# Performance work log

Hardware: AMD Instinct MI355X
Metric: run time of the kernel (lower is better)

Reference implementation:

```python
import jax, jax.numpy as jnp
import numpy as np

B, T, V, E, H, U = 32, 64, 32000, 300, 512, 512


def setup_inputs() -> dict:
    key = jax.random.key(0)
    ks = jax.random.split(key, 14)
    s = 0.05  # weight scale to keep gates in a sane range
    return {
        "trg_seq": jax.random.randint(ks[0], (B, T), 0, V, dtype=jnp.int32),
        "init_h": jax.random.normal(ks[1], (1, B, U), jnp.float32),
        "init_c": jax.random.normal(ks[2], (1, B, U), jnp.float32),
        "embedding": jax.random.normal(ks[3], (V, E), jnp.float32) * s,
        "Wh": jax.random.normal(ks[4], (H, U), jnp.float32) * s,
        "bh": jax.random.normal(ks[5], (H,), jnp.float32) * s,
        "Wc": jax.random.normal(ks[6], (H, U), jnp.float32) * s,
        "bc": jax.random.normal(ks[7], (H,), jnp.float32) * s,
        "W_ih": jax.random.normal(ks[8], (4 * H, E), jnp.float32) * s,
        "W_hh": jax.random.normal(ks[9], (4 * H, H), jnp.float32) * s,
        "b_ih": jax.random.normal(ks[10], (4 * H,), jnp.float32) * s,
        "b_hh": jax.random.normal(ks[11], (4 * H,), jnp.float32) * s,
        "W_logit": jax.random.normal(ks[12], (V, H), jnp.float32) * s,
        "b_logit": jax.random.normal(ks[13], (V,), jnp.float32) * s,
    }


def reference(trg_seq, init_h, init_c, embedding, Wh, bh, Wc, bc,
              W_ih, W_hh, b_ih, b_hh, W_logit, b_logit):
    # form_init: linear transform of encoder states -> LSTM initial h/c
    h0 = init_h[0] @ Wh.T + bh  # [B, H]
    c0 = init_c[0] @ Wc.T + bc  # [B, H]

    emb = embedding[trg_seq]                       # [B, T, E]
    x_gates = jnp.einsum('bte,ge->btg', emb, W_ih) + b_ih + b_hh  # [B, T, 4H]

    def step(carry, xg_t):
        h, c = carry
        gates = xg_t + h @ W_hh.T                  # [B, 4H]
        i, f, g, o = jnp.split(gates, 4, axis=-1)  # torch gate order i,f,g,o
        i, f, o = jax.nn.sigmoid(i), jax.nn.sigmoid(f), jax.nn.sigmoid(o)
        g = jnp.tanh(g)
        c = f * c + i * g
        h = o * jnp.tanh(c)
        return (h, c), h

    _, hs = jax.lax.scan(step, (h0, c0), x_gates.transpose(1, 0, 2))  # hs: [T, B, H]
    logits = jnp.tanh(hs) @ W_logit.T + b_logit    # [T, B, V]
    return logits.transpose(1, 0, 2)               # [B, T, V]
```

## Files before the change

kernel.cpp:

```cpp
#include <hip/hip_runtime.h>
#include <hip/hip_cooperative_groups.h>

typedef unsigned short u16;
typedef __attribute__((ext_vector_type(8))) unsigned short us8;
typedef __attribute__((ext_vector_type(8))) __bf16 bf16x8;
typedef __attribute__((ext_vector_type(4))) float f32x4;

#define B_ 32
#define T_ 64
#define V_ 32000
#define E_ 300
#define H_ 512
#define G4_ 2048
#define NBLK_ 32
#define NG_   224
#define NT_TILES 250
#define NM_TILES 16

__device__ __forceinline__ u16 f2b(float f){
  unsigned int x = __builtin_bit_cast(unsigned int, f);
  unsigned int r = (x + 0x7FFFu + ((x >> 16) & 1u)) >> 16;
  return (u16)r;
}
__device__ __forceinline__ float sigm(float x){ return 1.0f/(1.0f+expf(-x)); }

__device__ __forceinline__ void gload16(const u16* g, u16* l){
  __builtin_amdgcn_global_load_lds(
      (const __attribute__((address_space(1))) void*)g,
      (__attribute__((address_space(3))) void*)l, 16, 0, 0);
}

__global__ __launch_bounds__(256) void k_init(
    const float* __restrict__ init_h, const float* __restrict__ init_c,
    const float* __restrict__ Wh, const float* __restrict__ bh,
    const float* __restrict__ Wc, const float* __restrict__ bc,
    float* __restrict__ h0out, float* __restrict__ c0out,
    unsigned int* __restrict__ flag)
{
  if (blockIdx.x == 0){ flag[threadIdx.x] = 0u; flag[threadIdx.x + 256] = 0u; }
  int idx = blockIdx.x*blockDim.x + threadIdx.x;
  int sel = idx >> 14;
  int r = idx & 16383;
  int b = r >> 9, j = r & 511;
  const float* x = (sel ? init_c : init_h) + b*H_;
  const float* w = (sel ? Wc : Wh) + (size_t)j*H_;
  const float* bias = sel ? bc : bh;
  float acc = 0.f;
  for (int k = 0; k < H_; k += 8){
    f32x4 x0 = *(const f32x4*)(x + k), x1 = *(const f32x4*)(x + k + 4);
    f32x4 w0 = *(const f32x4*)(w + k), w1 = *(const f32x4*)(w + k + 4);
    acc += x0[0]*w0[0] + x0[1]*w0[1] + x0[2]*w0[2] + x0[3]*w0[3];
    acc += x1[0]*w1[0] + x1[1]*w1[1] + x1[2]*w1[2] + x1[3]*w1[3];
  }
  acc += bias[j];
  (sel ? c0out : h0out)[b*H_ + j] = acc;
}

__global__ __launch_bounds__(256) void k_cvt(
    const float* __restrict__ W, u16* __restrict__ W16)
{
  size_t i = ((size_t)blockIdx.x*256 + threadIdx.x)*8;
  f32x4 a = *(const f32x4*)(W + i);
  f32x4 b = *(const f32x4*)(W + i + 4);
  us8 u;
  u[0]=f2b(a[0]); u[1]=f2b(a[1]); u[2]=f2b(a[2]); u[3]=f2b(a[3]);
  u[4]=f2b(b[0]); u[5]=f2b(b[1]); u[6]=f2b(b[2]); u[7]=f2b(b[3]);
  *(us8*)(W16 + i) = u;
}

__global__ __launch_bounds__(256) void k_xgates(
    const float* __restrict__ emb, const float* __restrict__ Wih,
    const int* __restrict__ trg, const float* __restrict__ bih,
    const float* __restrict__ bhh, float* __restrict__ xg)
{
  __shared__ u16 As[128][40];
  __shared__ u16 Bs[128][40];
  const int bn0 = blockIdx.x*128, bm0 = blockIdx.y*128;
  const int tid = threadIdx.x;
  const int w = tid>>6, lane = tid&63;
  const int wr = w>>1, wc = w&1, lr = lane&15, lk = lane>>4;
  const int srow = tid>>1, half = tid&1;
  const int R = bm0 + srow;
  const int tt = R>>5, bb = R&31;
  const int token = trg[bb*T_ + tt];
  const float* arow = emb + (size_t)token*E_;
  const float* brow = Wih + (size_t)(bn0+srow)*E_;
  f32x4 acc[4][4] = {};
  for (int k0 = 0; k0 < E_; k0 += 32){
    int cbase = k0 + half*16;
    if (k0 + 32 <= E_){
      f32x4 a0=*(const f32x4*)(arow+cbase),    a1=*(const f32x4*)(arow+cbase+4);
      f32x4 a2=*(const f32x4*)(arow+cbase+8),  a3=*(const f32x4*)(arow+cbase+12);
      f32x4 b0=*(const f32x4*)(brow+cbase),    b1=*(const f32x4*)(brow+cbase+4);
      f32x4 b2=*(const f32x4*)(brow+cbase+8),  b3=*(const f32x4*)(brow+cbase+12);
      us8 ua, ub;
      ua[0]=f2b(a0[0]); ua[1]=f2b(a0[1]); ua[2]=f2b(a0[2]); ua[3]=f2b(a0[3]);
      ua[4]=f2b(a1[0]); ua[5]=f2b(a1[1]); ua[6]=f2b(a1[2]); ua[7]=f2b(a1[3]);
      ub[0]=f2b(a2[0]); ub[1]=f2b(a2[1]); ub[2]=f2b(a2[2]); ub[3]=f2b(a2[3]);
      ub[4]=f2b(a3[0]); ub[5]=f2b(a3[1]); ub[6]=f2b(a3[2]); ub[7]=f2b(a3[3]);
      *(us8*)&As[srow][half*16]   = ua;
      *(us8*)&As[srow][half*16+8] = ub;
      us8 va, vb;
      va[0]=f2b(b0[0]); va[1]=f2b(b0[1]); va[2]=f2b(b0[2]); va[3]=f2b(b0[3]);
      va[4]=f2b(b1[0]); va[5]=f2b(b1[1]); va[6]=f2b(b1[2]); va[7]=f2b(b1[3]);
      vb[0]=f2b(b2[0]); vb[1]=f2b(b2[1]); vb[2]=f2b(b2[2]); vb[3]=f2b(b2[3]);
      vb[4]=f2b(b3[0]); vb[5]=f2b(b3[1]); vb[6]=f2b(b3[2]); vb[7]=f2b(b3[3]);
      *(us8*)&Bs[srow][half*16]   = va;
      *(us8*)&Bs[srow][half*16+8] = vb;
    } else {
      for (int i = 0; i < 16; i++){
        int c = cbase + i;
        As[srow][half*16+i] = (c < E_) ? f2b(arow[c]) : (u16)0;
        Bs[srow][half*16+i] = (c < E_) ? f2b(brow[c]) : (u16)0;
      }
    }
    __syncthreads();
    bf16x8 af[4], bfr[4];
    #pragma unroll
    for (int m = 0; m < 4; m++) af[m] = *(const bf16x8*)&As[wr*64 + m*16 + lr][lk*8];
    #pragma unroll
    for (int n = 0; n < 4; n++) bfr[n] = *(const bf16x8*)&Bs[wc*64 + n*16 + lr][lk*8];
    #pragma unroll
    for (int m = 0; m < 4; m++)
      #pragma unroll
      for (int n = 0; n < 4; n++)
        acc[m][n] = __builtin_amdgcn_mfma_f32_16x16x32_bf16(af[m], bfr[n], acc[m][n], 0, 0, 0);
    __syncthreads();
  }
  #pragma unroll
  for (int n = 0; n < 4; n++){
    int col = bn0 + wc*64 + n*16 + lr;
    float bv = bih[col] + bhh[col];
    #pragma unroll
    for (int m = 0; m < 4; m++){
      #pragma unroll
      for (int i = 0; i < 4; i++){
        int row = bm0 + wr*64 + m*16 + lk*4 + i;
        xg[(size_t)row*G4_ + col] = acc[m][n][i] + bv;
      }
    }
  }
}

__global__ __launch_bounds__(512) void k_mega(
    const float* __restrict__ Whh, const float* __restrict__ xg,
    const float* __restrict__ h0, const float* __restrict__ c0,
    u16* __restrict__ h_g, u16* __restrict__ A_buf,
    unsigned int* __restrict__ flag,
    const u16* __restrict__ W16, const float* __restrict__ bias,
    float* __restrict__ out)
{
  __shared__ __align__(16) char smem[41472];
  const int tid = threadIdx.x;

  if (blockIdx.x < NBLK_){
    u16 (*hl)[520] = (u16(*)[520])smem;
    float (*gb)[32][16] = (float(*)[32][16])(smem + 33280);
    const int bj = blockIdx.x;
    const int wv = tid >> 6, lane = tid & 63;
    const int g = wv >> 1, m = wv & 1;
    const int lr = lane & 15, lk = lane >> 4;

    bf16x8 bw[16];
    {
      const float* wsrc = Whh + (size_t)(g*H_ + bj*16 + lr)*H_;
      #pragma unroll
      for (int ks = 0; ks < 16; ks++){
        f32x4 w0 = *(const f32x4*)(wsrc + ks*32 + lk*8);
        f32x4 w1 = *(const f32x4*)(wsrc + ks*32 + lk*8 + 4);
        us8 u;
        u[0]=f2b(w0[0]); u[1]=f2b(w0[1]); u[2]=f2b(w0[2]); u[3]=f2b(w0[3]);
        u[4]=f2b(w1[0]); u[5]=f2b(w1[1]); u[6]=f2b(w1[2]); u[7]=f2b(w1[3]);
        bw[ks] = __builtin_bit_cast(bf16x8, u);
      }
    }
    const int ub = tid >> 4, uj = tid & 15;
    float c_reg = c0[ub*H_ + bj*16 + uj];

    {
      int r = tid >> 4, seg = tid & 15;
      const float* src = h0 + r*H_ + seg*32;
      #pragma unroll
      for (int q = 0; q < 4; q++){
        f32x4 v0 = *(const f32x4*)(src + q*8);
        f32x4 v1 = *(const f32x4*)(src + q*8 + 4);
        us8 u;
        u[0]=f2b(v0[0]); u[1]=f2b(v0[1]); u[2]=f2b(v0[2]); u[3]=f2b(v0[3]);
        u[4]=f2b(v1[0]); u[5]=f2b(v1[1]); u[6]=f2b(v1[2]); u[7]=f2b(v1[3]);
        *(us8*)&hl[r][seg*32 + q*8] = u;
      }
    }
    __syncthreads();

    for (int t = 0; t < T_; t++){
      const float* xr = xg + (size_t)t*(B_*G4_) + ub*G4_ + bj*16 + uj;
      float x0 = xr[0*H_], x1 = xr[1*H_], x2 = xr[2*H_], x3 = xr[3*H_];

      f32x4 acc = {0.f, 0.f, 0.f, 0.f};
      #pragma unroll
      for (int ks = 0; ks < 16; ks++){
        bf16x8 a = *(const bf16x8*)&hl[m*16 + lr][ks*32 + lk*8];
        acc = __builtin_amdgcn_mfma_f32_16x16x32_bf16(a, bw[ks], acc, 0, 0, 0);
      }
      #pragma unroll
      for (int i = 0; i < 4; i++)
        gb[g][m*16 + lk*4 + i][lr] = acc[i];
      __syncthreads();

      float gi = sigm(gb[0][ub][uj] + x0);
      float gf = sigm(gb[1][ub][uj] + x1);
      float gg = tanhf(gb[2][ub][uj] + x2);
      float go = sigm(gb[3][ub][uj] + x3);
      c_reg = gf*c_reg + gi*gg;
      float h = go * tanhf(c_reg);
      int p = (t+1) & 1;
      h_g[p*(B_*H_) + bj*(B_*16) + tid] = f2b(h);

      __syncthreads();
      if (t < T_-1 && tid == 0)
        __hip_atomic_store(&flag[bj*16], (unsigned)(t+1),
                           __ATOMIC_RELEASE, __HIP_MEMORY_SCOPE_AGENT);

      A_buf[(size_t)t*(B_*H_) + ub*H_ + bj*16 + uj] = f2b(tanhf(h));
      if (t == T_-1) break;

      if (tid < 64){
        unsigned want = (unsigned)(t+1), guard = 0;
        while (__hip_atomic_load(&flag[(tid&31)*16], __ATOMIC_ACQUIRE,
                                 __HIP_MEMORY_SCOPE_AGENT) < want
               && guard < (1u<<18)) { __builtin_amdgcn_s_sleep(1); ++guard; }
      }
      __syncthreads();

      {
        int r = tid >> 4, seg = tid & 15;
        const u16* hb = h_g + p*(B_*H_);
        const u16* p0 = hb + (seg*2)  *(B_*16) + r*16;
        const u16* p1 = hb + (seg*2+1)*(B_*16) + r*16;
        us8 v0 = *(const us8*)(p0);
        us8 v1 = *(const us8*)(p0 + 8);
        us8 v2 = *(const us8*)(p1);
        us8 v3 = *(const us8*)(p1 + 8);
        *(us8*)&hl[r][seg*32]      = v0;
        *(us8*)&hl[r][seg*32 + 8]  = v1;
        *(us8*)&hl[r][seg*32 + 16] = v2;
        *(us8*)&hl[r][seg*32 + 24] = v3;
      }
      __syncthreads();
    }
    __syncthreads();
    if (tid == 0)
      __hip_atomic_store(&flag[bj*16], 65u,
                         __ATOMIC_RELEASE, __HIP_MEMORY_SCOPE_AGENT);
  } else {
    u16* As = (u16*)smem;
    u16* Bs = (u16*)(smem + 16384);
    const int w = tid>>6, lane = tid&63;
    const int wr = w & 1, wc = w >> 1;
    const int lr = lane&15, lk = lane>>4;
    const int r0 = w*8 + (lane>>3);
    const int r1 = 64 + r0;
    const int c0b = ((lane&7)*16) ^ ((r0&7)<<4);
    const int c1b = ((lane&7)*16) ^ ((r1&7)<<4);
    u16* adst0 = &As[(w*8)*64];
    u16* adst1 = &As[(64 + w*8)*64];
    u16* bdst0 = &Bs[(w*8)*64];
    u16* bdst1 = &Bs[(64 + w*8)*64];

    int prev_want = -1;
    for (int tile = (int)blockIdx.x - NBLK_; tile < NM_TILES*NT_TILES; tile += NG_){
      const int mt = tile / NT_TILES;
      const int nt = tile - mt*NT_TILES;
      const int bm0 = mt*128, bn0 = nt*128;
      const unsigned want = (mt < 15) ? (unsigned)(4*mt + 5) : 65u;
      if ((int)want != prev_want){
        if (tid < 64){
          unsigned guard = 0;
          for (;;){
            unsigned v = __hip_atomic_load(&flag[(tid&31)*16], __ATOMIC_RELAXED,
                                           __HIP_MEMORY_SCOPE_AGENT);
            if (__all(v >= want) || guard > (1u<<20)) break;
            __builtin_amdgcn_s_sleep(8); ++guard;
          }
          __builtin_amdgcn_fence(__ATOMIC_ACQUIRE, "agent");
        }
        prev_want = (int)want;
      }
      __syncthreads();

      const u16* a0p = A_buf + (size_t)(bm0+r0)*H_ + (c0b>>1);
      const u16* a1p = A_buf + (size_t)(bm0+r1)*H_ + (c1b>>1);
      const u16* b0p = W16   + (size_t)(bn0+r0)*H_ + (c0b>>1);
      const u16* b1p = W16   + (size_t)(bn0+r1)*H_ + (c1b>>1);
      f32x4 acc[4][2] = {};
      for (int k0 = 0; k0 < H_; k0 += 64){
        gload16(a0p + k0, adst0);
        gload16(a1p + k0, adst1);
        gload16(b0p + k0, bdst0);
        gload16(b1p + k0, bdst1);
        __syncthreads();
        #pragma unroll
        for (int s = 0; s < 2; s++){
          bf16x8 af[4], bfr[2];
          #pragma unroll
          for (int m = 0; m < 4; m++){
            int row = wr*64 + m*16 + lr;
            af[m] = *(const bf16x8*)((const char*)As + row*128
                       + ((s*64 + lk*16) ^ ((row&7)<<4)));
          }
          #pragma unroll
          for (int n = 0; n < 2; n++){
            int row = wc*32 + n*16 + lr;
            bfr[n] = *(const bf16x8*)((const char*)Bs + row*128
                       + ((s*64 + lk*16) ^ ((row&7)<<4)));
          }
          #pragma unroll
          for (int m = 0; m < 4; m++)
            #pragma unroll
            for (int n = 0; n < 2; n++)
              acc[m][n] = __builtin_amdgcn_mfma_f32_16x16x32_bf16(af[m], bfr[n], acc[m][n], 0, 0, 0);
        }
        __syncthreads();
      }
      #pragma unroll
      for (int n = 0; n < 2; n++){
        int col = bn0 + wc*32 + n*16 + lr;
        float bv = bias[col];
        #pragma unroll
        for (int m = 0; m < 4; m++){
          #pragma unroll
          for (int i = 0; i < 4; i++){
            int row = bm0 + wr*64 + m*16 + lk*4 + i;
            int t = row>>5, b = row&31;
            __builtin_nontemporal_store(acc[m][n][i] + bv,
                &out[(size_t)b*((size_t)T_*V_) + (size_t)t*V_ + col]);
          }
        }
      }
    }
  }
}

__global__ __launch_bounds__(512) void k_scan(
    const float* __restrict__ Whh, const float* __restrict__ xg,
    const float* __restrict__ h0, const float* __restrict__ c0,
    u16* __restrict__ h_g, u16* __restrict__ A_buf,
    unsigned int* __restrict__ flag)
{
  __shared__ u16 hl[32][520];
  __shared__ float gb[4][32][16];
  const int bj = blockIdx.x;
  const int tid = threadIdx.x;
  const int wv = tid >> 6, lane = tid & 63;
  const int g = wv >> 1, m = wv & 1;
  const int lr = lane & 15, lk = lane >> 4;
  bf16x8 bw[16];
  {
    const float* wsrc = Whh + (size_t)(g*H_ + bj*16 + lr)*H_;
    #pragma unroll
    for (int ks = 0; ks < 16; ks++){
      f32x4 w0 = *(const f32x4*)(wsrc + ks*32 + lk*8);
      f32x4 w1 = *(const f32x4*)(wsrc + ks*32 + lk*8 + 4);
      us8 u;
      u[0]=f2b(w0[0]); u[1]=f2b(w0[1]); u[2]=f2b(w0[2]); u[3]=f2b(w0[3]);
      u[4]=f2b(w1[0]); u[5]=f2b(w1[1]); u[6]=f2b(w1[2]); u[7]=f2b(w1[3]);
      bw[ks] = __builtin_bit_cast(bf16x8, u);
    }
  }
  const int ub = tid >> 4, uj = tid & 15;
  float c_reg = c0[ub*H_ + bj*16 + uj];
  {
    int r = tid >> 4, seg = tid & 15;
    const float* src = h0 + r*H_ + seg*32;
    #pragma unroll
    for (int q = 0; q < 4; q++){
      f32x4 v0 = *(const f32x4*)(src + q*8);
      f32x4 v1 = *(const f32x4*)(src + q*8 + 4);
      us8 u;
      u[0]=f2b(v0[0]); u[1]=f2b(v0[1]); u[2]=f2b(v0[2]); u[3]=f2b(v0[3]);
      u[4]=f2b(v1[0]); u[5]=f2b(v1[1]); u[6]=f2b(v1[2]); u[7]=f2b(v1[3]);
      *(us8*)&hl[r][seg*32 + q*8] = u;
    }
  }
  __syncthreads();
  for (int t = 0; t < T_; t++){
    const float* xr = xg + (size_t)t*(B_*G4_) + ub*G4_ + bj*16 + uj;
    float x0 = xr[0*H_], x1 = xr[1*H_], x2 = xr[2*H_], x3 = xr[3*H_];
    f32x4 acc = {0.f, 0.f, 0.f, 0.f};
    #pragma unroll
    for (int ks = 0; ks < 16; ks++){
      bf16x8 a = *(const bf16x8*)&hl[m*16 + lr][ks*32 + lk*8];
      acc = __builtin_amdgcn_mfma_f32_16x16x32_bf16(a, bw[ks], acc, 0, 0, 0);
    }
    #pragma unroll
    for (int i = 0; i < 4; i++)
      gb[g][m*16 + lk*4 + i][lr] = acc[i];
    __syncthreads();
    float gi = sigm(gb[0][ub][uj] + x0);
    float gf = sigm(gb[1][ub][uj] + x1);
    float gg = tanhf(gb[2][ub][uj] + x2);
    float go = sigm(gb[3][ub][uj] + x3);
    c_reg = gf*c_reg + gi*gg;
    float h = go * tanhf(c_reg);
    int p = (t+1) & 1;
    h_g[p*(B_*H_) + bj*(B_*16) + tid] = f2b(h);
    __syncthreads();
    if (t < T_-1 && tid == 0)
      __hip_atomic_store(&flag[bj*16], (unsigned)(t+1),
                         __ATOMIC_RELEASE, __HIP_MEMORY_SCOPE_AGENT);
    A_buf[(size_t)t*(B_*H_) + ub*H_ + bj*16 + uj] = f2b(tanhf(h));
    if (t == T_-1) break;
    if (tid < 64){
      unsigned want = (unsigned)(t+1), guard = 0;
      while (__hip_atomic_load(&flag[(tid&31)*16], __ATOMIC_ACQUIRE,
                               __HIP_MEMORY_SCOPE_AGENT) < want
             && guard < (1u<<18)) { __builtin_amdgcn_s_sleep(1); ++guard; }
    }
    __syncthreads();
    {
      int r = tid >> 4, seg = tid & 15;
      const u16* hb = h_g + p*(B_*H_);
      const u16* p0 = hb + (seg*2)  *(B_*16) + r*16;
      const u16* p1 = hb + (seg*2+1)*(B_*16) + r*16;
      us8 v0 = *(const us8*)(p0);
      us8 v1 = *(const us8*)(p0 + 8);
      us8 v2 = *(const us8*)(p1);
      us8 v3 = *(const us8*)(p1 + 8);
      *(us8*)&hl[r][seg*32]      = v0;
      *(us8*)&hl[r][seg*32 + 8]  = v1;
      *(us8*)&hl[r][seg*32 + 16] = v2;
      *(us8*)&hl[r][seg*32 + 24] = v3;
    }
    __syncthreads();
  }
}

__global__ __launch_bounds__(256) void k_logits16(
    const u16* __restrict__ A, const u16* __restrict__ W16,
    const float* __restrict__ bias, float* __restrict__ out)
{
  __shared__ u16 As[128*32];
  __shared__ u16 Bs[128*32];
  int bid = blockIdx.y*16 + blockIdx.x;
  int nbid = (bid & 7)*500 + (bid >> 3);
  const int bm0 = (nbid & 15)*128;
  const int bn0 = (nbid >> 4)*128;
  const int tid = threadIdx.x;
  const int w = tid>>6, lane = tid&63;
  const int wr = w>>1, wc = w&1, lr = lane&15, lk = lane>>4;
  const int srow = w*32 + (lane>>2);
  const int cb   = ((lane&3)*16) ^ (((srow>>1)&3)<<4);
  const u16* aptr = A   + (size_t)(bm0+srow)*H_ + (cb>>1);
  const u16* bptr = W16 + (size_t)(bn0+srow)*H_ + (cb>>1);
  u16* adst0 = &As[(w*32)*32];
  u16* adst1 = &As[(w*32+16)*32];
  u16* bdst0 = &Bs[(w*32)*32];
  u16* bdst1 = &Bs[(w*32+16)*32];
  f32x4 acc[4][4] = {};
  for (int k0 = 0; k0 < H_; k0 += 32){
    gload16(aptr + k0,          adst0);
    gload16(aptr + k0 + 16*H_,  adst1);
    gload16(bptr + k0,          bdst0);
    gload16(bptr + k0 + 16*H_,  bdst1);
    __syncthreads();
    bf16x8 af[4], bfr[4];
    #pragma unroll
    for (int m = 0; m < 4; m++){
      int row = wr*64 + m*16 + lr;
      af[m] = *(const bf16x8*)((const char*)As + row*64 + ((lk*16) ^ (((row>>1)&3)<<4)));
    }
    #pragma unroll
    for (int n = 0; n < 4; n++){
      int row = wc*64 + n*16 + lr;
      bfr[n] = *(const bf16x8*)((const char*)Bs + row*64 + ((lk*16) ^ (((row>>1)&3)<<4)));
    }
    #pragma unroll
    for (int m = 0; m < 4; m++)
      #pragma unroll
      for (int n = 0; n < 4; n++)
        acc[m][n] = __builtin_amdgcn_mfma_f32_16x16x32_bf16(af[m], bfr[n], acc[m][n], 0, 0, 0);
    __syncthreads();
  }
  #pragma unroll
  for (int n = 0; n < 4; n++){
    int col = bn0 + wc*64 + n*16 + lr;
    float bv = bias[col];
    #pragma unroll
    for (int m = 0; m < 4; m++){
      #pragma unroll
      for (int i = 0; i < 4; i++){
        int row = bm0 + wr*64 + m*16 + lk*4 + i;
        int t = row>>5, b = row&31;
        __builtin_nontemporal_store(acc[m][n][i] + bv,
            &out[(size_t)b*((size_t)T_*V_) + (size_t)t*V_ + col]);
      }
    }
  }
}

__global__ __launch_bounds__(256) void k_logits(
    const u16* __restrict__ A, const float* __restrict__ W,
    const float* __restrict__ bias, float* __restrict__ out)
{
  __shared__ u16 As[128][40];
  __shared__ u16 Bs[128][40];
  const int bm0 = blockIdx.x*128, bn0 = blockIdx.y*128;
  const int tid = threadIdx.x;
  const int w = tid>>6, lane = tid&63;
  const int wr = w>>1, wc = w&1, lr = lane&15, lk = lane>>4;
  const int srow = tid>>1, half = tid&1;
  const u16*   arow = A + (size_t)(bm0+srow)*H_;
  const float* brow = W + (size_t)(bn0+srow)*H_;
  f32x4 acc[4][4] = {};
  for (int k0 = 0; k0 < H_; k0 += 32){
    us8 a0 = *(const us8*)(arow + k0 + half*16);
    us8 a1 = *(const us8*)(arow + k0 + half*16 + 8);
    f32x4 b0 = *(const f32x4*)(brow + k0 + half*16);
    f32x4 b1 = *(const f32x4*)(brow + k0 + half*16 + 4);
    f32x4 b2 = *(const f32x4*)(brow + k0 + half*16 + 8);
    f32x4 b3 = *(const f32x4*)(brow + k0 + half*16 + 12);
    *(us8*)&As[srow][half*16]   = a0;
    *(us8*)&As[srow][half*16+8] = a1;
    us8 vb0, vb1;
    vb0[0]=f2b(b0[0]); vb0[1]=f2b(b0[1]); vb0[2]=f2b(b0[2]); vb0[3]=f2b(b0[3]);
    vb0[4]=f2b(b1[0]); vb0[5]=f2b(b1[1]); vb0[6]=f2b(b1[2]); vb0[7]=f2b(b1[3]);
    vb1[0]=f2b(b2[0]); vb1[1]=f2b(b2[1]); vb1[2]=f2b(b2[2]); vb1[3]=f2b(b2[3]);
    vb1[4]=f2b(b3[0]); vb1[5]=f2b(b3[1]); vb1[6]=f2b(b3[2]); vb1[7]=f2b(b3[3]);
    *(us8*)&Bs[srow][half*16]   = vb0;
    *(us8*)&Bs[srow][half*16+8] = vb1;
    __syncthreads();
    bf16x8 af[4], bfr[4];
    #pragma unroll
    for (int m = 0; m < 4; m++) af[m] = *(const bf16x8*)&As[wr*64 + m*16 + lr][lk*8];
    #pragma unroll
    for (int n = 0; n < 4; n++) bfr[n] = *(const bf16x8*)&Bs[wc*64 + n*16 + lr][lk*8];
    #pragma unroll
    for (int m = 0; m < 4; m++)
      #pragma unroll
      for (int n = 0; n < 4; n++)
        acc[m][n] = __builtin_amdgcn_mfma_f32_16x16x32_bf16(af[m], bfr[n], acc[m][n], 0, 0, 0);
    __syncthreads();
  }
  #pragma unroll
  for (int n = 0; n < 4; n++){
    int col = bn0 + wc*64 + n*16 + lr;
    float bv = bias[col];
    #pragma unroll
    for (int m = 0; m < 4; m++){
      #pragma unroll
      for (int i = 0; i < 4; i++){
        int row = bm0 + wr*64 + m*16 + lk*4 + i;
        int t = row>>5, b = row&31;
        out[(size_t)b*((size_t)T_*V_) + (size_t)t*V_ + col] = acc[m][n][i] + bv;
      }
    }
  }
}

extern "C" void kernel_launch(void* const* d_in, const int* in_sizes, int n_in,
                              void* d_out, int out_size, void* d_ws, size_t ws_size,
                              hipStream_t stream)
{
  const int*   trg    = (const int*)d_in[0];
  const float* init_h = (const float*)d_in[1];
  const float* init_c = (const float*)d_in[2];
  const float* emb    = (const float*)d_in[3];
  const float* Wh     = (const float*)d_in[4];
  const float* bh     = (const float*)d_in[5];
  const float* Wc     = (const float*)d_in[6];
  const float* bc     = (const float*)d_in[7];
  const float* Wih    = (const float*)d_in[8];
  const float* Whh    = (const float*)d_in[9];
  const float* bih    = (const float*)d_in[10];
  const float* bhh    = (const float*)d_in[11];
  const float* Wlogit = (const float*)d_in[12];
  const float* blogit = (const float*)d_in[13];
  float* out = (float*)d_out;

  char* ws = (char*)d_ws;
  float*        xg    = (float*)(ws);
  float*        h0    = (float*)(ws + 16777216);
  float*        c0    = (float*)(ws + 16842752);
  u16*          A_buf = (u16*)  (ws + 16908288);
  u16*          h_g   = (u16*)  (ws + 19005440);
  unsigned int* flag  = (unsigned int*)(ws + 19136512);
  u16*          W16   = (u16*)  (ws + 19138560);
  const size_t need_w16 = 19138560ull + 32768000ull;
  const bool use_w16 = (ws_size >= need_w16);

  hipLaunchKernelGGL(k_init, dim3(128), dim3(256), 0, stream,
                     init_h, init_c, Wh, bh, Wc, bc, h0, c0, flag);
  if (use_w16)
    hipLaunchKernelGGL(k_cvt, dim3((V_*H_)/(256*8)), dim3(256), 0, stream,
                       Wlogit, W16);
  hipLaunchKernelGGL(k_xgates, dim3(16, 16), dim3(256), 0, stream,
                     emb, Wih, trg, bih, bhh, xg);
  if (use_w16){
    void* args[] = { (void*)&Whh, (void*)&xg, (void*)&h0, (void*)&c0,
                     (void*)&h_g, (void*)&A_buf, (void*)&flag,
                     (void*)&W16, (void*)&blogit, (void*)&out };
    hipError_t merr = hipLaunchCooperativeKernel((void*)k_mega,
                          dim3(NBLK_ + NG_), dim3(512), args, 0, stream);
    if (merr != hipSuccess){
      void* sargs[] = { (void*)&Whh, (void*)&xg, (void*)&h0, (void*)&c0,
                        (void*)&h_g, (void*)&A_buf, (void*)&flag };
      hipLaunchCooperativeKernel((void*)k_scan, dim3(NBLK_), dim3(512),
                                 sargs, 0, stream);
      hipLaunchKernelGGL(k_logits16, dim3(16, 250), dim3(256), 0, stream,
                         A_buf, W16, blogit, out);
    }
  } else {
    void* args[] = { (void*)&Whh, (void*)&xg, (void*)&h0, (void*)&c0,
                     (void*)&h_g, (void*)&A_buf, (void*)&flag };
    hipLaunchCooperativeKernel((void*)k_scan, dim3(NBLK_), dim3(512), args, 0, stream);
    hipLaunchKernelGGL(k_logits, dim3(16, 250), dim3(256), 0, stream,
                       A_buf, Wlogit, blogit, out);
  }
}
```

Before: 439.5 us.

## Fuse weight conversion into xgates launch and pair M-tiles per logits tile

Folds the fp32-to-bf16 conversion of W_logit into the x-gates kernel as extra blocks, removing one kernel launch and letting the two independent jobs run concurrently. In the fused scan/logits megakernel, each consumer block now handles two consecutive M-tiles for the same N-tile. This keeps the W16 tile hot in cache and halves the tile-scheduling loop count. Pairing M-tiles can delay the start of the second tile's work until its scan flag is ready, which reduces how evenly work is spread across blocks.

```diff
diff --git a/kernel.cpp b/kernel.cpp
--- a/kernel.cpp
+++ b/kernel.cpp
@@ -56,27 +56,27 @@
   (sel ? c0out : h0out)[b*H_ + j] = acc;
 }
 
-__global__ __launch_bounds__(256) void k_cvt(
-    const float* __restrict__ W, u16* __restrict__ W16)
-{
-  size_t i = ((size_t)blockIdx.x*256 + threadIdx.x)*8;
-  f32x4 a = *(const f32x4*)(W + i);
-  f32x4 b = *(const f32x4*)(W + i + 4);
-  us8 u;
-  u[0]=f2b(a[0]); u[1]=f2b(a[1]); u[2]=f2b(a[2]); u[3]=f2b(a[3]);
-  u[4]=f2b(b[0]); u[5]=f2b(b[1]); u[6]=f2b(b[2]); u[7]=f2b(b[3]);
-  *(us8*)(W16 + i) = u;
-}
-
 __global__ __launch_bounds__(256) void k_xgates(
     const float* __restrict__ emb, const float* __restrict__ Wih,
     const int* __restrict__ trg, const float* __restrict__ bih,
-    const float* __restrict__ bhh, float* __restrict__ xg)
+    const float* __restrict__ bhh, float* __restrict__ xg,
+    const float* __restrict__ Wlogit, u16* __restrict__ W16)
 {
+  const int bid = blockIdx.x;
+  const int tid = threadIdx.x;
+  if (bid >= 256){
+    size_t i = ((size_t)(bid - 256)*256 + tid)*8;
+    f32x4 a = *(const f32x4*)(Wlogit + i);
+    f32x4 b = *(const f32x4*)(Wlogit + i + 4);
+    us8 u;
+    u[0]=f2b(a[0]); u[1]=f2b(a[1]); u[2]=f2b(a[2]); u[3]=f2b(a[3]);
+    u[4]=f2b(b[0]); u[5]=f2b(b[1]); u[6]=f2b(b[2]); u[7]=f2b(b[3]);
+    *(us8*)(W16 + i) = u;
+    return;
+  }
   __shared__ u16 As[128][40];
   __shared__ u16 Bs[128][40];
-  const int bn0 = blockIdx.x*128, bm0 = blockIdx.y*128;
-  const int tid = threadIdx.x;
+  const int bn0 = (bid & 15)*128, bm0 = (bid >> 4)*128;
   const int w = tid>>6, lane = tid&63;
   const int wr = w>>1, wc = w&1, lr = lane&15, lk = lane>>4;
   const int srow = tid>>1, half = tid&1;
@@ -268,72 +268,77 @@
     u16* bdst1 = &Bs[(64 + w*8)*64];
 
     int prev_want = -1;
-    for (int tile = (int)blockIdx.x - NBLK_; tile < NM_TILES*NT_TILES; tile += NG_){
-      const int mt = tile / NT_TILES;
-      const int nt = tile - mt*NT_TILES;
-      const int bm0 = mt*128, bn0 = nt*128;
-      const unsigned want = (mt < 15) ? (unsigned)(4*mt + 5) : 65u;
-      if ((int)want != prev_want){
-        if (tid < 64){
-          unsigned guard = 0;
-          for (;;){
-            unsigned v = __hip_atomic_load(&flag[(tid&31)*16], __ATOMIC_RELAXED,
-                                           __HIP_MEMORY_SCOPE_AGENT);
-            if (__all(v >= want) || guard > (1u<<20)) break;
-            __builtin_amdgcn_s_sleep(8); ++guard;
+    for (int pt = (int)blockIdx.x - NBLK_; pt < 8*NT_TILES; pt += NG_){
+      const int mt2 = pt / NT_TILES;
+      const int nt  = pt - mt2*NT_TILES;
+      const int bn0 = nt*128;
+      const u16* b0p = W16 + (size_t)(bn0+r0)*H_ + (c0b>>1);
+      const u16* b1p = W16 + (size_t)(bn0+r1)*H_ + (c1b>>1);
+      #pragma unroll
+      for (int hh = 0; hh < 2; hh++){
+        const int mt = 2*mt2 + hh;
+        const int bm0 = mt*128;
+        const unsigned want = (mt < 15) ? (unsigned)(4*mt + 5) : 65u;
+        if ((int)want != prev_want){
+          if (tid < 64){
+            unsigned guard = 0;
+            for (;;){
+              unsigned v = __hip_atomic_load(&flag[(tid&31)*16], __ATOMIC_RELAXED,
+                                             __HIP_MEMORY_SCOPE_AGENT);
+              if (__all(v >= want) || guard > (1u<<20)) break;
+              __builtin_amdgcn_s_sleep(8); ++guard;
+            }
+            __builtin_amdgcn_fence(__ATOMIC_ACQUIRE, "agent");
           }
-          __builtin_amdgcn_fence(__ATOMIC_ACQUIRE, "agent");
+          prev_want = (int)want;
         }
-        prev_want = (int)want;
-      }
-      __syncthreads();
-
-      const u16* a0p = A_buf + (size_t)(bm0+r0)*H_ + (c0b>>1);
-      const u16* a1p = A_buf + (size_t)(bm0+r1)*H_ + (c1b>>1);
-      const u16* b0p = W16   + (size_t)(bn0+r0)*H_ + (c0b>>1);
-      const u16* b1p = W16   + (size_t)(bn0+r1)*H_ + (c1b>>1);
-      f32x4 acc[4][2] = {};
-      for (int k0 = 0; k0 < H_; k0 += 64){
-        gload16(a0p + k0, adst0);
-        gload16(a1p + k0, adst1);
-        gload16(b0p + k0, bdst0);
-        gload16(b1p + k0, bdst1);
         __syncthreads();
+
+        const u16* a0p = A_buf + (size_t)(bm0+r0)*H_ + (c0b>>1);
+        const u16* a1p = A_buf + (size_t)(bm0+r1)*H_ + (c1b>>1);
+        f32x4 acc[4][2] = {};
+        for (int k0 = 0; k0 < H_; k0 += 64){
+          gload16(a0p + k0, adst0);
+          gload16(a1p + k0, adst1);
+          gload16(b0p + k0, bdst0);
+          gload16(b1p + k0, bdst1);
+          __syncthreads();
+          #pragma unroll
+          for (int s = 0; s < 2; s++){
+            bf16x8 af[4], bfr[2];
+            #pragma unroll
+            for (int m = 0; m < 4; m++){
+              int row = wr*64 + m*16 + lr;
+              af[m] = *(const bf16x8*)((const char*)As + row*128
+                         + ((s*64 + lk*16) ^ ((row&7)<<4)));
+            }
+            #pragma unroll
+            for (int n = 0; n < 2; n++){
+              int row = wc*32 + n*16 + lr;
+              bfr[n] = *(const bf16x8*)((const char*)Bs + row*128
+                         + ((s*64 + lk*16) ^ ((row&7)<<4)));
+            }
+            #pragma unroll
+            for (int m = 0; m < 4; m++)
+              #pragma unroll
+              for (int n = 0; n < 2; n++)
+                acc[m][n] = __builtin_amdgcn_mfma_f32_16x16x32_bf16(af[m], bfr[n], acc[m][n], 0, 0, 0);
+          }
+          __syncthreads();
+        }
         #pragma unroll
-        for (int s = 0; s < 2; s++){
-          bf16x8 af[4], bfr[2];
+        for (int n = 0; n < 2; n++){
+          int col = bn0 + wc*32 + n*16 + lr;
+          float bv = bias[col];
           #pragma unroll
           for (int m = 0; m < 4; m++){
-            int row = wr*64 + m*16 + lr;
-            af[m] = *(const bf16x8*)((const char*)As + row*128
-                       + ((s*64 + lk*16) ^ ((row&7)<<4)));
-          }
-          #pragma unroll
-          for (int n = 0; n < 2; n++){
-            int row = wc*32 + n*16 + lr;
-            bfr[n] = *(const bf16x8*)((const char*)Bs + row*128
-                       + ((s*64 + lk*16) ^ ((row&7)<<4)));
-          }
-          #pragma unroll
-          for (int m = 0; m < 4; m++)
             #pragma unroll
-            for (int n = 0; n < 2; n++)
-              acc[m][n] = __builtin_amdgcn_mfma_f32_16x16x32_bf16(af[m], bfr[n], acc[m][n], 0, 0, 0);
-        }
-        __syncthreads();
-      }
-      #pragma unroll
-      for (int n = 0; n < 2; n++){
-        int col = bn0 + wc*32 + n*16 + lr;
-        float bv = bias[col];
-        #pragma unroll
-        for (int m = 0; m < 4; m++){
-          #pragma unroll
-          for (int i = 0; i < 4; i++){
-            int row = bm0 + wr*64 + m*16 + lk*4 + i;
-            int t = row>>5, b = row&31;
-            __builtin_nontemporal_store(acc[m][n][i] + bv,
-                &out[(size_t)b*((size_t)T_*V_) + (size_t)t*V_ + col]);
+            for (int i = 0; i < 4; i++){
+              int row = bm0 + wr*64 + m*16 + lk*4 + i;
+              int t = row>>5, b = row&31;
+              __builtin_nontemporal_store(acc[m][n][i] + bv,
+                  &out[(size_t)b*((size_t)T_*V_) + (size_t)t*V_ + col]);
+            }
           }
         }
       }
@@ -590,11 +595,8 @@
 
   hipLaunchKernelGGL(k_init, dim3(128), dim3(256), 0, stream,
                      init_h, init_c, Wh, bh, Wc, bc, h0, c0, flag);
-  if (use_w16)
-    hipLaunchKernelGGL(k_cvt, dim3((V_*H_)/(256*8)), dim3(256), 0, stream,
-                       Wlogit, W16);
-  hipLaunchKernelGGL(k_xgates, dim3(16, 16), dim3(256), 0, stream,
-                     emb, Wih, trg, bih, bhh, xg);
+  hipLaunchKernelGGL(k_xgates, dim3(use_w16 ? 8256 : 256), dim3(256), 0, stream,
+                     emb, Wih, trg, bih, bhh, xg, Wlogit, W16);
   if (use_w16){
     void* args[] = { (void*)&Whh, (void*)&xg, (void*)&h0, (void*)&c0,
                      (void*)&h_g, (void*)&A_buf, (void*)&flag,
```

Result: no change. 437.0 us (median of 2 runs) (-0.6%).
